# Performance work log

Measured on AMD Instinct MI355X. Metric: run time of the kernel, lower is better.

## Reference

```python
import jax, jax.numpy as jnp
import numpy as np

IN_FEAT = 3 * 32 * 32  # channels*height*width
HID = 1024
CLASSES = 10
EPS = 1e-5


def binarize(w):
    # Deterministic BinaryConnect: sign(w) in {-1, +1} (sign(0) -> +1)
    return jnp.where(w >= 0, 1.0, -1.0).astype(w.dtype)


def batchnorm(h, gamma, beta):
    # training-mode BatchNorm1d: biased batch stats over batch axis
    mean = jnp.mean(h, axis=0)
    var = jnp.var(h, axis=0)
    return gamma * (h - mean) * jax.lax.rsqrt(var + EPS) + beta


def setup_inputs() -> dict:
    key = jax.random.key(0)
    ks = jax.random.split(key, 6)
    x = jax.random.normal(ks[0], (8192, 3, 32, 32), dtype=jnp.float32)
    # latent real-valued weights, torch Linear layout [out, in], kaiming-ish scale
    W1 = jax.random.normal(ks[1], (HID, IN_FEAT), dtype=jnp.float32) * (1.0 / np.sqrt(IN_FEAT))
    W2 = jax.random.normal(ks[2], (HID, HID), dtype=jnp.float32) * (1.0 / np.sqrt(HID))
    W3 = jax.random.normal(ks[3], (HID, HID), dtype=jnp.float32) * (1.0 / np.sqrt(HID))
    W4 = jax.random.normal(ks[4], (CLASSES, HID), dtype=jnp.float32) * (1.0 / np.sqrt(HID))
    g1 = jnp.ones((HID,), jnp.float32); b1 = jnp.zeros((HID,), jnp.float32)
    g2 = jnp.ones((HID,), jnp.float32); b2 = jnp.zeros((HID,), jnp.float32)
    g3 = jnp.ones((HID,), jnp.float32); b3 = jnp.zeros((HID,), jnp.float32)
    return {"x": x, "W1": W1, "W2": W2, "W3": W3, "W4": W4,
            "g1": g1, "b1": b1, "g2": g2, "b2": b2, "g3": g3, "b3": b3}


def reference(x, W1, W2, W3, W4, g1, b1, g2, b2, g3, b3):
    h = x.reshape(-1, IN_FEAT)                       # [B, 3072]
    h = jax.nn.relu(h @ binarize(W1).T)              # [B, 1024]
    h = batchnorm(h, g1, b1)
    h = jax.nn.relu(h @ binarize(W2).T)
    h = batchnorm(h, g2, b2)
    h = jax.nn.relu(h @ binarize(W3).T)
    h = batchnorm(h, g3, b3)
    return h @ binarize(W4).T                        # [B, classes]
```

## Files before the change

### kernel.cpp

```cpp
#include <hip/hip_runtime.h>
#include <stdint.h>

typedef unsigned short u16;
typedef __attribute__((ext_vector_type(8))) unsigned short ushort8;
typedef __attribute__((ext_vector_type(8))) __bf16 bf16x8;
typedef __attribute__((ext_vector_type(4))) float f32x4;

__device__ __forceinline__ u16 f2bf(float f) {
    union { float f; unsigned int u; } v; v.f = f;
    unsigned int r = v.u + 0x7FFFu + ((v.u >> 16) & 1u);
    return (u16)(r >> 16);
}
__device__ __forceinline__ float bf2f(u16 b) {
    union { unsigned int u; float f; } v; v.u = ((unsigned int)b) << 16;
    return v.f;
}

typedef __attribute__((address_space(1))) const uint32_t* gptr_t;
typedef __attribute__((address_space(3))) uint32_t* lptr_t;
__device__ __forceinline__ void async_copy16(const void* g, void* l) {
    __builtin_amdgcn_global_load_lds((gptr_t)g, (lptr_t)l, 16, 0, 0);
}


__global__ __launch_bounds__(256) void f32_to_bf16_kernel(
    const float* __restrict__ in, u16* __restrict__ out, int n8)
{
    int i = blockIdx.x * 256 + threadIdx.x;
    if (i >= n8) return;
    const float4* p = (const float4*)(in + (size_t)i * 8);
    float4 x0 = p[0], x1 = p[1];
    ushort8 o;
    o[0] = f2bf(x0.x); o[1] = f2bf(x0.y); o[2] = f2bf(x0.z); o[3] = f2bf(x0.w);
    o[4] = f2bf(x1.x); o[5] = f2bf(x1.y); o[6] = f2bf(x1.z); o[7] = f2bf(x1.w);
    *(ushort8*)(out + (size_t)i * 8) = o;
}

__global__ __launch_bounds__(256) void binarize_kernel(
    const float* __restrict__ in, u16* __restrict__ out, int n8)
{
    int i = blockIdx.x * 256 + threadIdx.x;
    if (i >= n8) return;
    const float4* p = (const float4*)(in + (size_t)i * 8);
    float4 x0 = p[0], x1 = p[1];
    ushort8 o;
    o[0] = x0.x >= 0.f ? 0x3F80 : 0xBF80;
    o[1] = x0.y >= 0.f ? 0x3F80 : 0xBF80;
    o[2] = x0.z >= 0.f ? 0x3F80 : 0xBF80;
    o[3] = x0.w >= 0.f ? 0x3F80 : 0xBF80;
    o[4] = x1.x >= 0.f ? 0x3F80 : 0xBF80;
    o[5] = x1.y >= 0.f ? 0x3F80 : 0xBF80;
    o[6] = x1.z >= 0.f ? 0x3F80 : 0xBF80;
    o[7] = x1.w >= 0.f ? 0x3F80 : 0xBF80;
    *(ushort8*)(out + (size_t)i * 8) = o;
}

__global__ __launch_bounds__(256) void build_w4t(
    const float* __restrict__ W4, u16* __restrict__ W4T)
{
    int idx = blockIdx.x * 256 + threadIdx.x;
    int k = idx >> 4, c = idx & 15;
    u16 v = 0;
    if (c < 10) v = (W4[(size_t)c * 1024 + k] >= 0.f) ? 0x3F80 : 0xBF80;
    W4T[idx] = v;
}


__global__ __launch_bounds__(256) void gemm_bt_relu_bn(
    const u16* __restrict__ A, const u16* __restrict__ B,
    u16* __restrict__ H, int M, int N, int K)
{
    __shared__ __align__(16) u16 As[2][128 * 64];
    __shared__ __align__(16) u16 Bs[2][128 * 64];

    const int tid  = threadIdx.x;
    const int wid  = tid >> 6;
    const int lane = tid & 63;
    const int lr   = lane & 15;
    const int hk   = lane >> 4;
    const int x7   = lr & 7;
    const int wr   = wid >> 1;
    const int wc   = wid & 1;
    const int row0 = blockIdx.x * 128;
    const int col0 = blockIdx.y * 128;

    const int s_r = tid >> 3;
    const int s_c = (((tid & 7) ^ (s_r & 7)) << 3);
    const u16* gA = A + (size_t)(row0 + s_r) * K + s_c;
    const u16* gB = B + (size_t)(col0 + s_r) * K + s_c;

    int a_base[4], b_base[4];
    #pragma unroll
    for (int i = 0; i < 4; ++i) a_base[i] = (wr * 64 + i * 16 + lr) * 64;
    #pragma unroll
    for (int j = 0; j < 4; ++j) b_base[j] = (wc * 64 + j * 16 + lr) * 64;
    const int xs0 = ((hk)     ^ x7) << 3;
    const int xs1 = ((hk + 4) ^ x7) << 3;

    f32x4 acc[4][4];
    #pragma unroll
    for (int i = 0; i < 4; ++i)
        #pragma unroll
        for (int j = 0; j < 4; ++j)
            acc[i][j] = (f32x4){0.f, 0.f, 0.f, 0.f};

    const int NT = K >> 6;

    auto STAGE = [&](int buf, int t) {
        const u16* pa = gA + (size_t)t * 64;
        const u16* pb = gB + (size_t)t * 64;
        #pragma unroll
        for (int i = 0; i < 4; ++i)
            async_copy16(pa + (size_t)i * 32 * K, &As[buf][i * 2048 + wid * 512]);
        #pragma unroll
        for (int i = 0; i < 4; ++i)
            async_copy16(pb + (size_t)i * 32 * K, &Bs[buf][i * 2048 + wid * 512]);
    };

    STAGE(0, 0);
    STAGE(1, 1);

    for (int t = 0; t < NT; ++t) {
        const int buf = t & 1;
        if (t + 1 < NT) asm volatile("s_waitcnt vmcnt(8)" ::: "memory");
        else            asm volatile("s_waitcnt vmcnt(0)" ::: "memory");
        __builtin_amdgcn_s_barrier();

        bf16x8 af[4][2], bg[4][2];
        #pragma unroll
        for (int i = 0; i < 4; ++i) {
            af[i][0] = *(const bf16x8*)&As[buf][a_base[i] + xs0];
            af[i][1] = *(const bf16x8*)&As[buf][a_base[i] + xs1];
        }
        #pragma unroll
        for (int j = 0; j < 4; ++j) {
            bg[j][0] = *(const bf16x8*)&Bs[buf][b_base[j] + xs0];
            bg[j][1] = *(const bf16x8*)&Bs[buf][b_base[j] + xs1];
        }
        asm volatile("s_waitcnt lgkmcnt(0)" ::: "memory");
        __builtin_amdgcn_sched_barrier(0);
        __builtin_amdgcn_s_barrier();

        if (t + 2 < NT) STAGE(buf, t + 2);

        __builtin_amdgcn_s_setprio(1);
        #pragma unroll
        for (int kk = 0; kk < 2; ++kk)
            #pragma unroll
            for (int i = 0; i < 4; ++i)
                #pragma unroll
                for (int j = 0; j < 4; ++j)
                    acc[i][j] = __builtin_amdgcn_mfma_f32_16x16x32_bf16(
                        af[i][kk], bg[j][kk], acc[i][j], 0, 0, 0);
        __builtin_amdgcn_s_setprio(0);
    }

    const int er = hk * 4;
    #pragma unroll
    for (int i = 0; i < 4; ++i) {
        #pragma unroll
        for (int j = 0; j < 4; ++j) {
            int r = row0 + wr * 64 + i * 16 + er;
            int c = col0 + wc * 64 + j * 16 + lr;
            #pragma unroll
            for (int b2 = 0; b2 < 4; ++b2) {
                float x = acc[i][j][b2];
                x = x > 0.f ? x : 0.f;
                H[(size_t)(r + b2) * N + c] = f2bf(x);
            }
        }
    }
}


__global__ __launch_bounds__(256) void bn_partial(
    const u16* __restrict__ H, float* __restrict__ part)
{
    int c  = blockIdx.x * 256 + threadIdx.x;
    int r0 = blockIdx.y * 64;
    float s = 0.f, s2 = 0.f;
    #pragma unroll 8
    for (int r = 0; r < 64; ++r) {
        float v = bf2f(H[(size_t)(r0 + r) * 1024 + c]);
        s += v; s2 += v * v;
    }
    part[(size_t)blockIdx.y * 1024 + c] = s;
    part[131072 + (size_t)blockIdx.y * 1024 + c] = s2;
}

__global__ __launch_bounds__(256) void bn_finalize(
    const float* __restrict__ part, const float* __restrict__ gamma,
    const float* __restrict__ beta, float* __restrict__ ss)
{
    int c = blockIdx.x * 256 + threadIdx.x;
    float s = 0.f, s2 = 0.f;
    for (int i = 0; i < 128; ++i) {
        s  += part[(size_t)i * 1024 + c];
        s2 += part[131072 + (size_t)i * 1024 + c];
    }
    float mean = s * (1.0f / 8192.0f);
    float var  = fmaxf(s2 * (1.0f / 8192.0f) - mean * mean, 0.f);
    float sc   = gamma[c] * rsqrtf(var + 1e-5f);
    ss[c]        = sc;
    ss[1024 + c] = beta[c] - mean * sc;
}

__global__ __launch_bounds__(256) void bn_apply(
    const u16* __restrict__ H, const float* __restrict__ ss,
    u16* __restrict__ Aout)
{
    int i = blockIdx.x * 256 + threadIdx.x;
    int c = (i * 8) & 1023;
    ushort8 h = *(const ushort8*)(H + (size_t)i * 8);
    float4 sc0 = *(const float4*)(ss + c);
    float4 sc1 = *(const float4*)(ss + c + 4);
    float4 sh0 = *(const float4*)(ss + 1024 + c);
    float4 sh1 = *(const float4*)(ss + 1024 + c + 4);
    ushort8 o;
    o[0] = f2bf(bf2f(h[0]) * sc0.x + sh0.x);
    o[1] = f2bf(bf2f(h[1]) * sc0.y + sh0.y);
    o[2] = f2bf(bf2f(h[2]) * sc0.z + sh0.z);
    o[3] = f2bf(bf2f(h[3]) * sc0.w + sh0.w);
    o[4] = f2bf(bf2f(h[4]) * sc1.x + sh1.x);
    o[5] = f2bf(bf2f(h[5]) * sc1.y + sh1.y);
    o[6] = f2bf(bf2f(h[6]) * sc1.z + sh1.z);
    o[7] = f2bf(bf2f(h[7]) * sc1.w + sh1.w);
    *(ushort8*)(Aout + (size_t)i * 8) = o;
}


__global__ __launch_bounds__(256) void head_kernel(
    const u16* __restrict__ A, const u16* __restrict__ W4T,
    float* __restrict__ out)
{
    const int lane = threadIdx.x & 63;
    const int wid  = threadIdx.x >> 6;
    const int r    = blockIdx.x * 4 + wid;

    float acc[10];
    #pragma unroll
    for (int c = 0; c < 10; c++) acc[c] = 0.f;

    #pragma unroll
    for (int j = 0; j < 16; ++j) {
        int k = j * 64 + lane;
        float a = bf2f(A[(size_t)r * 1024 + k]);
        ushort8 w0 = *(const ushort8*)(W4T + (size_t)k * 16);
        acc[0] += a * bf2f(w0[0]); acc[1] += a * bf2f(w0[1]);
        acc[2] += a * bf2f(w0[2]); acc[3] += a * bf2f(w0[3]);
        acc[4] += a * bf2f(w0[4]); acc[5] += a * bf2f(w0[5]);
        acc[6] += a * bf2f(w0[6]); acc[7] += a * bf2f(w0[7]);
        u16 w8 = W4T[(size_t)k * 16 + 8];
        u16 w9 = W4T[(size_t)k * 16 + 9];
        acc[8] += a * bf2f(w8);    acc[9] += a * bf2f(w9);
    }
    #pragma unroll
    for (int c = 0; c < 10; c++) {
        float s = acc[c];
        #pragma unroll
        for (int off = 32; off > 0; off >>= 1) s += __shfl_xor(s, off, 64);
        acc[c] = s;
    }
    if (lane == 0) {
        #pragma unroll
        for (int c = 0; c < 10; c++) out[(size_t)r * 10 + c] = acc[c];
    }
}


extern "C" void kernel_launch(void* const* d_in, const int* in_sizes, int n_in,
                              void* d_out, int out_size, void* d_ws, size_t ws_size,
                              hipStream_t stream) {
    const float* x  = (const float*)d_in[0];
    const float* W1 = (const float*)d_in[1];
    const float* W2 = (const float*)d_in[2];
    const float* W3 = (const float*)d_in[3];
    const float* W4 = (const float*)d_in[4];
    const float* g1 = (const float*)d_in[5];
    const float* b1 = (const float*)d_in[6];
    const float* g2 = (const float*)d_in[7];
    const float* b2 = (const float*)d_in[8];
    const float* g3 = (const float*)d_in[9];
    const float* b3 = (const float*)d_in[10];
    float* out = (float*)d_out;

    char* ws = (char*)d_ws;
    u16*   Xb   = (u16*)  (ws + 0);
    u16*   Hb   = (u16*)  (ws + 50331648);
    u16*   W1b  = (u16*)  (ws + 67108864);
    u16*   W2b  = (u16*)  (ws + 73400320);
    u16*   W3b  = (u16*)  (ws + 75497472);
    u16*   W4T  = (u16*)  (ws + 77594624);
    float* part = (float*)(ws + 77627392);
    float* ss   = (float*)(ws + 78675968);
    u16*   A    = Xb;

    f32_to_bf16_kernel<<<12288, 256, 0, stream>>>(x, Xb, 3145728);
    binarize_kernel<<<1536, 256, 0, stream>>>(W1, W1b, 393216);
    binarize_kernel<<<512, 256, 0, stream>>>(W2, W2b, 131072);
    binarize_kernel<<<512, 256, 0, stream>>>(W3, W3b, 131072);
    build_w4t<<<64, 256, 0, stream>>>(W4, W4T);

    dim3 gemm_grid(64, 8);
    dim3 bn_grid(4, 128);

    gemm_bt_relu_bn<<<gemm_grid, 256, 0, stream>>>(Xb, W1b, Hb, 8192, 1024, 3072);
    bn_partial<<<bn_grid, 256, 0, stream>>>(Hb, part);
    bn_finalize<<<4, 256, 0, stream>>>(part, g1, b1, ss);
    bn_apply<<<4096, 256, 0, stream>>>(Hb, ss, A);

    gemm_bt_relu_bn<<<gemm_grid, 256, 0, stream>>>(A, W2b, Hb, 8192, 1024, 1024);
    bn_partial<<<bn_grid, 256, 0, stream>>>(Hb, part);
    bn_finalize<<<4, 256, 0, stream>>>(part, g2, b2, ss);
    bn_apply<<<4096, 256, 0, stream>>>(Hb, ss, A);

    gemm_bt_relu_bn<<<gemm_grid, 256, 0, stream>>>(A, W3b, Hb, 8192, 1024, 1024);
    bn_partial<<<bn_grid, 256, 0, stream>>>(Hb, part);
    bn_finalize<<<4, 256, 0, stream>>>(part, g3, b3, ss);
    bn_apply<<<4096, 256, 0, stream>>>(Hb, ss, A);

    head_kernel<<<2048, 256, 0, stream>>>(A, W4T, out);
}
```

Baseline: 211.2 us.

## Fold BatchNorm into next-layer weights and fuse batch stats into GEMM epilogue

Computes per-column sum and sum-of-squares inside the GEMM epilogue, which removes the separate bn_partial pass over H. The BN scale is folded into the binarized weights of the next layer and the shift into a per-output bias, so the bn_apply pass over the activations disappears. The head applies the last BN inline. In exchange the weights are no longer exact ±1 in bf16: the scale is rounded into them, which changes numerics slightly. The activation buffer now ping-pongs between two buffers, and bias2/bias3 reuse the Xb region once it is dead.

Result: faster. 191.1 us (-9.5%).

```diff
diff --git a/kernel.cpp b/kernel.cpp
--- a/kernel.cpp
+++ b/kernel.cpp
@@ -3,6 +3,7 @@
 
 typedef unsigned short u16;
 typedef __attribute__((ext_vector_type(8))) unsigned short ushort8;
+typedef __attribute__((ext_vector_type(4))) unsigned short ushort4v;
 typedef __attribute__((ext_vector_type(8))) __bf16 bf16x8;
 typedef __attribute__((ext_vector_type(4))) float f32x4;
 
@@ -65,10 +66,40 @@
     W4T[idx] = v;
 }
 
-
-__global__ __launch_bounds__(256) void gemm_bt_relu_bn(
+__global__ __launch_bounds__(256) void rescale_w(
+    const float* __restrict__ W, const float* __restrict__ ss,
+    u16* __restrict__ Wp, float* __restrict__ bias)
+{
+    const int lane = threadIdx.x & 63;
+    const int wid  = threadIdx.x >> 6;
+    const int r    = blockIdx.x * 4 + wid;
+    float bsum = 0.f;
+    #pragma unroll
+    for (int k0 = 0; k0 < 1024; k0 += 256) {
+        int k = k0 + lane * 4;
+        float4 w  = *(const float4*)(W + (size_t)r * 1024 + k);
+        float4 sc = *(const float4*)(ss + k);
+        float4 sh = *(const float4*)(ss + 1024 + k);
+        ushort4v o;
+        o[0] = f2bf(w.x >= 0.f ? sc.x : -sc.x);
+        o[1] = f2bf(w.y >= 0.f ? sc.y : -sc.y);
+        o[2] = f2bf(w.z >= 0.f ? sc.z : -sc.z);
+        o[3] = f2bf(w.w >= 0.f ? sc.w : -sc.w);
+        bsum += (w.x >= 0.f ? sh.x : -sh.x) + (w.y >= 0.f ? sh.y : -sh.y)
+              + (w.z >= 0.f ? sh.z : -sh.z) + (w.w >= 0.f ? sh.w : -sh.w);
+        *(ushort4v*)(Wp + (size_t)r * 1024 + k) = o;
+    }
+    #pragma unroll
+    for (int off = 32; off; off >>= 1) bsum += __shfl_xor(bsum, off, 64);
+    if (lane == 0) bias[r] = bsum;
+}
+
+
+__global__ __launch_bounds__(256) void gemm_fused(
     const u16* __restrict__ A, const u16* __restrict__ B,
-    u16* __restrict__ H, int M, int N, int K)
+    u16* __restrict__ H, const float* __restrict__ bias,
+    float* __restrict__ partS, float* __restrict__ partS2,
+    int M, int N, int K)
 {
     __shared__ __align__(16) u16 As[2][128 * 64];
     __shared__ __align__(16) u16 Bs[2][128 * 64];
@@ -157,46 +188,42 @@
 
     const int er = hk * 4;
     #pragma unroll
-    for (int i = 0; i < 4; ++i) {
-        #pragma unroll
-        for (int j = 0; j < 4; ++j) {
-            int r = row0 + wr * 64 + i * 16 + er;
-            int c = col0 + wc * 64 + j * 16 + lr;
+    for (int j = 0; j < 4; ++j) {
+        const int c = col0 + wc * 64 + j * 16 + lr;
+        const float bj = bias ? bias[c] : 0.f;
+        float s = 0.f, s2 = 0.f;
+        #pragma unroll
+        for (int i = 0; i < 4; ++i) {
+            const int r = row0 + wr * 64 + i * 16 + er;
             #pragma unroll
             for (int b2 = 0; b2 < 4; ++b2) {
-                float x = acc[i][j][b2];
+                float x = acc[i][j][b2] + bj;
                 x = x > 0.f ? x : 0.f;
+                s += x; s2 += x * x;
                 H[(size_t)(r + b2) * N + c] = f2bf(x);
             }
         }
-    }
-}
-
-
-__global__ __launch_bounds__(256) void bn_partial(
-    const u16* __restrict__ H, float* __restrict__ part)
-{
-    int c  = blockIdx.x * 256 + threadIdx.x;
-    int r0 = blockIdx.y * 64;
-    float s = 0.f, s2 = 0.f;
-    #pragma unroll 8
-    for (int r = 0; r < 64; ++r) {
-        float v = bf2f(H[(size_t)(r0 + r) * 1024 + c]);
-        s += v; s2 += v * v;
-    }
-    part[(size_t)blockIdx.y * 1024 + c] = s;
-    part[131072 + (size_t)blockIdx.y * 1024 + c] = s2;
-}
+        s  += __shfl_xor(s, 16, 64);  s  += __shfl_xor(s, 32, 64);
+        s2 += __shfl_xor(s2, 16, 64); s2 += __shfl_xor(s2, 32, 64);
+        if (hk == 0) {
+            const int p = blockIdx.x * 2 + wr;
+            partS [(size_t)p * 1024 + c] = s;
+            partS2[(size_t)p * 1024 + c] = s2;
+        }
+    }
+}
+
 
 __global__ __launch_bounds__(256) void bn_finalize(
-    const float* __restrict__ part, const float* __restrict__ gamma,
-    const float* __restrict__ beta, float* __restrict__ ss)
+    const float* __restrict__ partS, const float* __restrict__ partS2,
+    const float* __restrict__ gamma, const float* __restrict__ beta,
+    float* __restrict__ ss)
 {
     int c = blockIdx.x * 256 + threadIdx.x;
     float s = 0.f, s2 = 0.f;
     for (int i = 0; i < 128; ++i) {
-        s  += part[(size_t)i * 1024 + c];
-        s2 += part[131072 + (size_t)i * 1024 + c];
+        s  += partS [(size_t)i * 1024 + c];
+        s2 += partS2[(size_t)i * 1024 + c];
     }
     float mean = s * (1.0f / 8192.0f);
     float var  = fmaxf(s2 * (1.0f / 8192.0f) - mean * mean, 0.f);
@@ -205,33 +232,10 @@
     ss[1024 + c] = beta[c] - mean * sc;
 }
 
-__global__ __launch_bounds__(256) void bn_apply(
-    const u16* __restrict__ H, const float* __restrict__ ss,
-    u16* __restrict__ Aout)
-{
-    int i = blockIdx.x * 256 + threadIdx.x;
-    int c = (i * 8) & 1023;
-    ushort8 h = *(const ushort8*)(H + (size_t)i * 8);
-    float4 sc0 = *(const float4*)(ss + c);
-    float4 sc1 = *(const float4*)(ss + c + 4);
-    float4 sh0 = *(const float4*)(ss + 1024 + c);
-    float4 sh1 = *(const float4*)(ss + 1024 + c + 4);
-    ushort8 o;
-    o[0] = f2bf(bf2f(h[0]) * sc0.x + sh0.x);
-    o[1] = f2bf(bf2f(h[1]) * sc0.y + sh0.y);
-    o[2] = f2bf(bf2f(h[2]) * sc0.z + sh0.z);
-    o[3] = f2bf(bf2f(h[3]) * sc0.w + sh0.w);
-    o[4] = f2bf(bf2f(h[4]) * sc1.x + sh1.x);
-    o[5] = f2bf(bf2f(h[5]) * sc1.y + sh1.y);
-    o[6] = f2bf(bf2f(h[6]) * sc1.z + sh1.z);
-    o[7] = f2bf(bf2f(h[7]) * sc1.w + sh1.w);
-    *(ushort8*)(Aout + (size_t)i * 8) = o;
-}
-
 
 __global__ __launch_bounds__(256) void head_kernel(
-    const u16* __restrict__ A, const u16* __restrict__ W4T,
-    float* __restrict__ out)
+    const u16* __restrict__ H, const u16* __restrict__ W4T,
+    const float* __restrict__ ss, float* __restrict__ out)
 {
     const int lane = threadIdx.x & 63;
     const int wid  = threadIdx.x >> 6;
@@ -244,7 +248,7 @@
     #pragma unroll
     for (int j = 0; j < 16; ++j) {
         int k = j * 64 + lane;
-        float a = bf2f(A[(size_t)r * 1024 + k]);
+        float a = fmaf(bf2f(H[(size_t)r * 1024 + k]), ss[k], ss[1024 + k]);
         ushort8 w0 = *(const ushort8*)(W4T + (size_t)k * 16);
         acc[0] += a * bf2f(w0[0]); acc[1] += a * bf2f(w0[1]);
         acc[2] += a * bf2f(w0[2]); acc[3] += a * bf2f(w0[3]);
@@ -285,39 +289,35 @@
     float* out = (float*)d_out;
 
     char* ws = (char*)d_ws;
-    u16*   Xb   = (u16*)  (ws + 0);
-    u16*   Hb   = (u16*)  (ws + 50331648);
-    u16*   W1b  = (u16*)  (ws + 67108864);
-    u16*   W2b  = (u16*)  (ws + 73400320);
-    u16*   W3b  = (u16*)  (ws + 75497472);
-    u16*   W4T  = (u16*)  (ws + 77594624);
-    float* part = (float*)(ws + 77627392);
-    float* ss   = (float*)(ws + 78675968);
-    u16*   A    = Xb;
+    u16*   Xb    = (u16*)  (ws + 0);
+    float* bias2 = (float*)(ws + 0);
+    float* bias3 = (float*)(ws + 4096);
+    u16*   Hb0   = (u16*)  (ws + 50331648);
+    u16*   Hb1   = (u16*)  (ws + 67108864);
+    u16*   W1b   = (u16*)  (ws + 83886080);
+    u16*   W2p   = (u16*)  (ws + 90177536);
+    u16*   W3p   = (u16*)  (ws + 92274688);
+    u16*   W4T   = (u16*)  (ws + 94371840);
+    float* partS = (float*)(ws + 94404608);
+    float* partS2= (float*)(ws + 94928896);
+    float* ss    = (float*)(ws + 95453184);
 
     f32_to_bf16_kernel<<<12288, 256, 0, stream>>>(x, Xb, 3145728);
     binarize_kernel<<<1536, 256, 0, stream>>>(W1, W1b, 393216);
-    binarize_kernel<<<512, 256, 0, stream>>>(W2, W2b, 131072);
-    binarize_kernel<<<512, 256, 0, stream>>>(W3, W3b, 131072);
     build_w4t<<<64, 256, 0, stream>>>(W4, W4T);
 
     dim3 gemm_grid(64, 8);
-    dim3 bn_grid(4, 128);
-
-    gemm_bt_relu_bn<<<gemm_grid, 256, 0, stream>>>(Xb, W1b, Hb, 8192, 1024, 3072);
-    bn_partial<<<bn_grid, 256, 0, stream>>>(Hb, part);
-    bn_finalize<<<4, 256, 0, stream>>>(part, g1, b1, ss);
-    bn_apply<<<4096, 256, 0, stream>>>(Hb, ss, A);
-
-    gemm_bt_relu_bn<<<gemm_grid, 256, 0, stream>>>(A, W2b, Hb, 8192, 1024, 1024);
-    bn_partial<<<bn_grid, 256, 0, stream>>>(Hb, part);
-    bn_finalize<<<4, 256, 0, stream>>>(part, g2, b2, ss);
-    bn_apply<<<4096, 256, 0, stream>>>(Hb, ss, A);
-
-    gemm_bt_relu_bn<<<gemm_grid, 256, 0, stream>>>(A, W3b, Hb, 8192, 1024, 1024);
-    bn_partial<<<bn_grid, 256, 0, stream>>>(Hb, part);
-    bn_finalize<<<4, 256, 0, stream>>>(part, g3, b3, ss);
-    bn_apply<<<4096, 256, 0, stream>>>(Hb, ss, A);
-
-    head_kernel<<<2048, 256, 0, stream>>>(A, W4T, out);
-}
+
+    gemm_fused<<<gemm_grid, 256, 0, stream>>>(Xb, W1b, Hb0, nullptr, partS, partS2, 8192, 1024, 3072);
+    bn_finalize<<<4, 256, 0, stream>>>(partS, partS2, g1, b1, ss);
+    rescale_w<<<256, 256, 0, stream>>>(W2, ss, W2p, bias2);
+
+    gemm_fused<<<gemm_grid, 256, 0, stream>>>(Hb0, W2p, Hb1, bias2, partS, partS2, 8192, 1024, 1024);
+    bn_finalize<<<4, 256, 0, stream>>>(partS, partS2, g2, b2, ss);
+    rescale_w<<<256, 256, 0, stream>>>(W3, ss, W3p, bias3);
+
+    gemm_fused<<<gemm_grid, 256, 0, stream>>>(Hb1, W3p, Hb0, bias3, partS, partS2, 8192, 1024, 1024);
+    bn_finalize<<<4, 256, 0, stream>>>(partS, partS2, g3, b3, ss);
+
+    head_kernel<<<2048, 256, 0, stream>>>(Hb0, W4T, ss, out);
+}
```
